# Kernel tuning notes

Measured on AMD Instinct MI355X. Metric: run time of the kernel, lower is better.

Reference implementation:

```python
import jax, jax.numpy as jnp
import numpy as np

# Module/config constants (match init_kwargs and torch forward defaults, octaves=8)
H, W, B = 1024, 1024, 16
OCTAVES = 8
PERSISTENCE = 0.5
LACUNARITY = 2.0
EXPONENT = 4.0
SCALE = 100.0
EVOLUTION = 0.1
FRAME = 0
BRIGHTNESS = 0.0
CONTRAST = 0.0
MIN_CLAMP = 0.0
MAX_CLAMP = 1.0
P_COUNT = max(H, W) ** 2  # permutation table size (doubled via concat)


def _fade(t):
    # 6t^5 - 15t^4 + 10t^3, Horner form
    return t * t * t * (t * (t * 6.0 - 15.0) + 10.0)


def _lerp(t, a, b):
    return a + t * (b - a)


def _grad(h, x, y, z):
    h = h & 15
    u = jnp.where(h < 8, x, y)
    v = jnp.where(h < 4, y, jnp.where((h == 12) | (h == 14), x, z))
    return jnp.where((h & 1) == 0, u, -u) + jnp.where((h & 2) == 0, v, -v)


def _noise(x, y, z, p):
    # classic 3D Perlin noise; x:(1,W), y:(H,1), z:(1,) broadcast to (H,W)
    Xi = (jnp.floor(x) % 255).astype(jnp.int32)
    Yi = (jnp.floor(y) % 255).astype(jnp.int32)
    Zi = (jnp.floor(z) % 255).astype(jnp.int32)
    xf = x - jnp.floor(x)
    yf = y - jnp.floor(y)
    zf = z - jnp.floor(z)
    u = _fade(xf)
    v = _fade(yf)
    w = _fade(zf)
    A = p[Xi] + Yi            # (H,W)
    AA = p[A] + Zi
    AB = p[A + 1] + Zi
    Bc = p[Xi + 1] + Yi
    BA = p[Bc] + Zi
    BB = p[Bc + 1] + Zi
    x1 = _lerp(u, _grad(p[AA], xf, yf, zf), _grad(p[BA], xf - 1, yf, zf))
    x2 = _lerp(u, _grad(p[AB], xf, yf - 1, zf), _grad(p[BB], xf - 1, yf - 1, zf))
    x3 = _lerp(u, _grad(p[AA + 1], xf, yf, zf - 1), _grad(p[BA + 1], xf - 1, yf, zf - 1))
    x4 = _lerp(u, _grad(p[AB + 1], xf, yf - 1, zf - 1), _grad(p[BB + 1], xf - 1, yf - 1, zf - 1))
    return _lerp(w, _lerp(v, x1, x2), _lerp(v, x3, x4))


def _forward(p_all, X, Y, Z):
    xs = jnp.arange(W, dtype=jnp.float32)[None, :] + X  # (1,W)
    ys = jnp.arange(H, dtype=jnp.float32)[:, None] + Y  # (H,1)

    def one_image(p, b):
        z0 = EVOLUTION * b + Z + FRAME  # (1,)
        acc = jnp.zeros((H, W), jnp.float32)
        for o in range(OCTAVES):  # small fixed loop over octaves
            freq = LACUNARITY ** o
            amp = PERSISTENCE ** o
            nz = (z0 + FRAME * EVOLUTION) / SCALE * freq
            n = _noise(xs / SCALE * freq, ys / SCALE * freq, nz, p)
            # noise * amp**exponent accumulated with weight amp -> amp**(exponent+1)
            acc = acc + n * np.float32(amp ** EXPONENT * amp)
        mn, mx = acc.min(), acc.max()
        img = (acc - mn) / (mx - mn) * (MAX_CLAMP - MIN_CLAMP) + MIN_CLAMP
        # second range_normalize(x) with None targets is the identity
        return (img + BRIGHTNESS) * (1.0 + CONTRAST)

    imgs = jax.vmap(one_image)(p_all, jnp.arange(B, dtype=jnp.float32))  # (B,H,W)
    return imgs[..., None]  # (B,H,W,1)


def setup_inputs() -> dict:
    key = jax.random.key(0)
    keys = jax.random.split(key, B)
    perm = jax.vmap(lambda k: jax.random.permutation(k, P_COUNT))(keys).astype(jnp.int32)
    p_all = jnp.concatenate([perm, perm], axis=1)  # (B, 2*P_COUNT), torch .repeat(2)
    kx, ky, kz = jax.random.split(jax.random.fold_in(key, 1), 3)
    X = jax.random.uniform(kx, (1,), jnp.float32, 0.0, 1000.0)
    Y = jax.random.uniform(ky, (1,), jnp.float32, 0.0, 1000.0)
    Z = jax.random.uniform(kz, (1,), jnp.float32, 0.0, 100.0)
    return {"p_all": p_all, "X": X, "Y": Y, "Z": Z}


def reference(p_all, X, Y, Z):
    return _forward(p_all, X, Y, Z)
```

## Files before the change

kernel.cpp:

```cpp
#include <hip/hip_runtime.h>


#define HW  1048576
#define PSTRIDE 2097152
#define PBS 1049088
#define OCT 4
#define RPB 8

struct ZTab { float zf, w; int Zi, pad; float w0, w1, wz0, wz1; };

__device__ __forceinline__ float fadef(float t) {
    return t * t * t * (t * (t * 6.0f - 15.0f) + 10.0f);
}
__device__ __forceinline__ void gdec(int h, float& a, float& cy, float& cz) {
    float s1 = (h & 1) ? -1.f : 1.f;
    float s2 = (h & 2) ? -1.f : 1.f;
    bool  vx = (h == 12) || (h == 14);
    a  = ((h < 8) ? s1 : 0.f) + (vx ? s2 : 0.f);
    cy = ((h >= 8) ? s1 : 0.f) + ((h < 4) ? s2 : 0.f);
    cz = (h >= 4 && !vx) ? s2 : 0.f;
}

__constant__ const float AW[8] = {
    1.0f, 0.03125f, 9.765625e-4f, 3.0517578125e-5f,
    9.5367431640625e-7f, 2.9802322387695312e-8f,
    9.313225746154785e-10f, 2.9103830456733704e-11f
};

__global__ void ppf_k0(const float* __restrict__ Z, ZTab* __restrict__ zs) {
    int t = threadIdx.x;
    if (t < 128) {
        int b = t >> 3, o = t & 7;
        float z0 = 0.1f * (float)b + Z[0];
        float freq = (float)(1 << o);
        float nz = (z0 / 100.0f) * freq;
        float fz = floorf(nz);
        ZTab zt;
        zt.Zi = ((int)fz) % 255;
        zt.zf = nz - fz;
        zt.w  = fadef(zt.zf);
        zt.pad = 0;
        zt.w0 = 1.0f - zt.w;
        zt.w1 = zt.w;
        zt.wz0 = zt.w0 * zt.zf;
        zt.wz1 = zt.w1 * (zt.zf - 1.0f);
        zs[t] = zt;
    }
}

__global__ void ppf_k0b(const int* __restrict__ p_all, unsigned char* __restrict__ pb) {
    int idx = blockIdx.x * 256 + threadIdx.x;
    int b = blockIdx.y;
    if (idx < PBS / 4) {
        int4 v = ((const int4*)(p_all + (size_t)b * PSTRIDE))[idx];
        uchar4 o;
        o.x = (unsigned char)(v.x & 15);
        o.y = (unsigned char)(v.y & 15);
        o.z = (unsigned char)(v.z & 15);
        o.w = (unsigned char)(v.w & 15);
        ((uchar4*)(pb + (size_t)b * PBS))[idx] = o;
    }
}

template <int USE_PB>
__global__ void ppf_k1(const int* __restrict__ p_all, const unsigned char* __restrict__ pb,
                       const ZTab* __restrict__ zs, unsigned char* __restrict__ G) {
    int i = threadIdx.x;
    int j = blockIdx.x;
    int b = blockIdx.y;
    const int* p = p_all + (size_t)b * PSTRIDE;
    const unsigned char* pbb = pb + (size_t)b * PBS;
    int pi = p[i];
    int q  = p[pi + j];
    size_t gbase = (size_t)b * OCT * 65536 + (size_t)j * 256 + i;
#pragma unroll
    for (int o = 0; o < OCT; o++) {
        int Zi = zs[b * 8 + o].Zi;
        int h0, h1;
        if (USE_PB) {
            h0 = pbb[q + Zi];
            h1 = pbb[q + Zi + 1];
        } else {
            h0 = p[q + Zi] & 15;
            h1 = p[q + Zi + 1] & 15;
        }
        G[gbase + (size_t)o * 65536] = (unsigned char)(h0 | (h1 << 4));
    }
}

__launch_bounds__(256, 8)
__global__ void ppf_k2(const unsigned char* __restrict__ G,
                       const ZTab* __restrict__ zs,
                       const float* __restrict__ X, const float* __restrict__ Y,
                       float* __restrict__ out, float2* __restrict__ pmm) {
    __shared__ __align__(16) float2 CT[2][OCT * 256];
    __shared__ float red[8];

    const int tid = threadIdx.x;
    const int bx = blockIdx.x, b = blockIdx.y;
    const float X0 = X[0], Y0 = Y[0];

    float zw0[OCT], zw1[OCT], zwz0[OCT], zwz1[OCT];
#pragma unroll
    for (int o = 0; o < OCT; o++) {
        ZTab z = zs[b * 8 + o];
        zw0[o] = z.w0; zw1[o] = z.w1; zwz0[o] = z.wz0; zwz1[o] = z.wz1;
    }

    float txs[4];
#pragma unroll
    for (int i = 0; i < 4; i++) txs[i] = ((float)(tid + 256 * i) + X0) * 0.01f;

    float mnr = 1e30f, mxr = -1e30f;
    int cur = 0;

    for (int rr = 0; rr < RPB; rr++) {
        const int r = bx * RPB + rr;
        const float ty = ((float)r + Y0) * 0.01f;

#pragma unroll
        for (int o = 0; o < OCT; o++) {
            float y  = ty * (float)(1 << o);
            float fy = floorf(y);
            float yf = y - fy, ym1 = yf - 1.0f;
            float v  = fadef(yf);
            int iy = (int)fy;
            int Yi = (iy >= 255) ? iy - 255 : iy;
            const unsigned char* gro = G + (((size_t)(b * OCT + o)) << 16)
                                         + (unsigned)Yi * 256u + tid;
            int byt0 = gro[0];
            int byt1 = gro[256];
            float a0, cy0, cz0, a1, cy1, cz1;
            gdec(byt0 & 15, a0, cy0, cz0);
            gdec(byt0 >> 4, a1, cy1, cz1);
            float A_0  = fmaf(zw1[o],  a1,  zw0[o] * a0);
            float CY_0 = fmaf(zw1[o],  cy1, zw0[o] * cy0);
            float CZ_0 = fmaf(zwz1[o], cz1, zwz0[o] * cz0);
            gdec(byt1 & 15, a0, cy0, cz0);
            gdec(byt1 >> 4, a1, cy1, cz1);
            float A_1  = fmaf(zw1[o],  a1,  zw0[o] * a0);
            float CY_1 = fmaf(zw1[o],  cy1, zw0[o] * cy0);
            float CZ_1 = fmaf(zwz1[o], cz1, zwz0[o] * cz0);
            float CA = A_0 + v * (A_1 - A_0);
            float B0 = fmaf(CY_0, yf,  CZ_0);
            float B1 = fmaf(CY_1, ym1, CZ_1);
            float CB = B0 + v * (B1 - B0);
            float aw = AW[o];
            CT[cur][o * 256 + tid] = make_float2(CA * aw, CB * aw);
        }
        __syncthreads();

        float accv[4] = {0.f, 0.f, 0.f, 0.f};
#pragma unroll
        for (int o = 0; o < OCT; o++) {
            const float fr = (float)(1 << o);
            const float2* cto = CT[cur] + o * 256;
            float xfv[4], uv[4];
            float2 c0v[4], c1v[4];
#pragma unroll
            for (int i = 0; i < 4; i++) {
                float x  = txs[i] * fr;
                float fx = floorf(x);
                float xf = x - fx;
                int  ix  = (int)fx;
                int  s   = (ix >> 8) + (ix & 255);
                s -= (s >= 255) ? 255 : 0;
                xfv[i] = xf;
                uv[i]  = fadef(xf);
                c0v[i] = cto[s];
                c1v[i] = cto[s + 1];
            }
#pragma unroll
            for (int i = 0; i < 4; i++) {
                float P = fmaf(c0v[i].x, xfv[i], c0v[i].y);
                float Q = fmaf(c1v[i].x, xfv[i] - 1.0f, c1v[i].y);
                accv[i] += fmaf(uv[i], Q - P, P);
            }
        }

        size_t obase = ((size_t)b << 20) + ((size_t)r << 10) + tid;
#pragma unroll
        for (int i = 0; i < 4; i++) out[obase + 256 * i] = accv[i];
        mnr = fminf(mnr, fminf(fminf(accv[0], accv[1]), fminf(accv[2], accv[3])));
        mxr = fmaxf(mxr, fmaxf(fmaxf(accv[0], accv[1]), fmaxf(accv[2], accv[3])));

        cur ^= 1;
    }

#pragma unroll
    for (int off = 32; off > 0; off >>= 1) {
        mnr = fminf(mnr, __shfl_down(mnr, off));
        mxr = fmaxf(mxr, __shfl_down(mxr, off));
    }
    if ((tid & 63) == 0) { red[2 * (tid >> 6)] = mnr; red[2 * (tid >> 6) + 1] = mxr; }
    __syncthreads();
    if (tid == 0) {
        float mn = fminf(fminf(red[0], red[2]), fminf(red[4], red[6]));
        float mx = fmaxf(fmaxf(red[1], red[3]), fmaxf(red[5], red[7]));
        pmm[b * 128 + bx] = make_float2(mn, mx);
    }
}

__global__ void ppf_k2b(const float2* __restrict__ pmm, float* __restrict__ mmf) {
    int b = blockIdx.x, t = threadIdx.x;
    __shared__ float s[4];
    float2 v = pmm[b * 128 + t];
    float mn = v.x, mx = v.y;
#pragma unroll
    for (int off = 32; off > 0; off >>= 1) {
        mn = fminf(mn, __shfl_down(mn, off));
        mx = fmaxf(mx, __shfl_down(mx, off));
    }
    if ((t & 63) == 0) { s[(t >> 6) * 2] = mn; s[(t >> 6) * 2 + 1] = mx; }
    __syncthreads();
    if (t == 0) {
        mn = fminf(s[0], s[2]);
        mx = fmaxf(s[1], s[3]);
        mmf[2 * b]     = mn;
        mmf[2 * b + 1] = 1.0f / (mx - mn);
    }
}

__global__ void ppf_k3(float* __restrict__ out, const float* __restrict__ mmf) {
    int b = blockIdx.y;
    int idx = blockIdx.x * 256 + threadIdx.x;
    float mn = mmf[2 * b];
    float s  = mmf[2 * b + 1];
    float4* o4 = (float4*)(out + (size_t)b * HW);
    float4 v = o4[idx];
    v.x = (v.x - mn) * s;
    v.y = (v.y - mn) * s;
    v.z = (v.z - mn) * s;
    v.w = (v.w - mn) * s;
    o4[idx] = v;
}

extern "C" void kernel_launch(void* const* d_in, const int* in_sizes, int n_in,
                              void* d_out, int out_size, void* d_ws, size_t ws_size,
                              hipStream_t stream) {
    const int*   p_all = (const int*)d_in[0];
    const float* X     = (const float*)d_in[1];
    const float* Y     = (const float*)d_in[2];
    const float* Z     = (const float*)d_in[3];
    float* out = (float*)d_out;
    char* ws = (char*)d_ws;

    const size_t GSZ = (size_t)16 * OCT * 65536;
    const size_t OFF_PB = GSZ;
    const size_t OFF_ZS_FULL = OFF_PB + (size_t)16 * PBS;
    const size_t NEED_FULL   = OFF_ZS_FULL + 8192 + 4096 + 16384;
    bool full = (ws_size >= NEED_FULL);
    size_t off_zs = full ? OFF_ZS_FULL : OFF_PB;

    unsigned char* G  = (unsigned char*)ws;
    unsigned char* pb = (unsigned char*)(ws + OFF_PB);
    ZTab*   zs        = (ZTab*)  (ws + off_zs);
    float*  mmf       = (float*) (ws + off_zs + 8192);
    float2* pmm       = (float2*)(ws + off_zs + 8192 + 4096);

    ppf_k0<<<1, 128, 0, stream>>>(Z, zs);
    if (full) {
        ppf_k0b<<<dim3(1025, 16), 256, 0, stream>>>(p_all, pb);
        ppf_k1<1><<<dim3(256, 16), 256, 0, stream>>>(p_all, pb, zs, G);
    } else {
        ppf_k1<0><<<dim3(256, 16), 256, 0, stream>>>(p_all, pb, zs, G);
    }
    ppf_k2<<<dim3(128, 16), 256, 0, stream>>>(G, zs, X, Y, out, pmm);
    ppf_k2b<<<16, 128, 0, stream>>>(pmm, mmf);
    ppf_k3<<<dim3(1024, 16), 256, 0, stream>>>(out, mmf);
}
```

Before: 367.5 us.

## Pack hash pairs, interleave octave bytes, drop modulo wrap, fuse min-max finalize

```diff
diff --git a/kernel.cpp b/kernel.cpp
--- a/kernel.cpp
+++ b/kernel.cpp
@@ -48,48 +48,49 @@
     }
 }
 
-__global__ void ppf_k0b(const int* __restrict__ p_all, unsigned char* __restrict__ pb) {
+__global__ void ppf_k0b(const int* __restrict__ p_all, unsigned char* __restrict__ pbp) {
     int idx = blockIdx.x * 256 + threadIdx.x;
     int b = blockIdx.y;
     if (idx < PBS / 4) {
-        int4 v = ((const int4*)(p_all + (size_t)b * PSTRIDE))[idx];
+        const int* p = p_all + (size_t)b * PSTRIDE;
+        int4 v = ((const int4*)p)[idx];
+        int n4 = p[idx * 4 + 4];
         uchar4 o;
-        o.x = (unsigned char)(v.x & 15);
-        o.y = (unsigned char)(v.y & 15);
-        o.z = (unsigned char)(v.z & 15);
-        o.w = (unsigned char)(v.w & 15);
-        ((uchar4*)(pb + (size_t)b * PBS))[idx] = o;
-    }
-}
-
-template <int USE_PB>
-__global__ void ppf_k1(const int* __restrict__ p_all, const unsigned char* __restrict__ pb,
-                       const ZTab* __restrict__ zs, unsigned char* __restrict__ G) {
-    int i = threadIdx.x;
-    int j = blockIdx.x;
+        o.x = (unsigned char)((v.x & 15) | ((v.y & 15) << 4));
+        o.y = (unsigned char)((v.y & 15) | ((v.z & 15) << 4));
+        o.z = (unsigned char)((v.z & 15) | ((v.w & 15) << 4));
+        o.w = (unsigned char)((v.w & 15) | ((n4 & 15) << 4));
+        ((uchar4*)(pbp + (size_t)b * PBS))[idx] = o;
+    }
+}
+
+template <int USE_PBP>
+__global__ void ppf_k1(const int* __restrict__ p_all, const unsigned char* __restrict__ pbp,
+                       const ZTab* __restrict__ zs, unsigned* __restrict__ G2) {
+    int j = threadIdx.x;
+    int i = blockIdx.x;
     int b = blockIdx.y;
     const int* p = p_all + (size_t)b * PSTRIDE;
-    const unsigned char* pbb = pb + (size_t)b * PBS;
     int pi = p[i];
     int q  = p[pi + j];
-    size_t gbase = (size_t)b * OCT * 65536 + (size_t)j * 256 + i;
+    const unsigned char* pp = pbp + (size_t)b * PBS;
+    unsigned w = 0;
 #pragma unroll
     for (int o = 0; o < OCT; o++) {
         int Zi = zs[b * 8 + o].Zi;
-        int h0, h1;
-        if (USE_PB) {
-            h0 = pbb[q + Zi];
-            h1 = pbb[q + Zi + 1];
+        unsigned byt;
+        if (USE_PBP) {
+            byt = pp[q + Zi];
         } else {
-            h0 = p[q + Zi] & 15;
-            h1 = p[q + Zi + 1] & 15;
+            byt = (unsigned)((p[q + Zi] & 15) | ((p[q + Zi + 1] & 15) << 4));
         }
-        G[gbase + (size_t)o * 65536] = (unsigned char)(h0 | (h1 << 4));
-    }
+        w |= byt << (8 * o);
+    }
+    G2[((size_t)b << 16) + ((unsigned)j << 8) + (unsigned)i] = w;
 }
 
 __launch_bounds__(256, 8)
-__global__ void ppf_k2(const unsigned char* __restrict__ G,
+__global__ void ppf_k2(const unsigned* __restrict__ G2,
                        const ZTab* __restrict__ zs,
                        const float* __restrict__ X, const float* __restrict__ Y,
                        float* __restrict__ out, float2* __restrict__ pmm) {
@@ -111,6 +112,8 @@
 #pragma unroll
     for (int i = 0; i < 4; i++) txs[i] = ((float)(tid + 256 * i) + X0) * 0.01f;
 
+    const unsigned char* gb = (const unsigned char*)G2 + ((size_t)b << 18);
+
     float mnr = 1e30f, mxr = -1e30f;
     int cur = 0;
 
@@ -124,12 +127,10 @@
             float fy = floorf(y);
             float yf = y - fy, ym1 = yf - 1.0f;
             float v  = fadef(yf);
-            int iy = (int)fy;
-            int Yi = (iy >= 255) ? iy - 255 : iy;
-            const unsigned char* gro = G + (((size_t)(b * OCT + o)) << 16)
-                                         + (unsigned)Yi * 256u + tid;
+            int Yi = (int)fy;
+            const unsigned char* gro = gb + ((((unsigned)Yi << 8) + tid) << 2) + o;
             int byt0 = gro[0];
-            int byt1 = gro[256];
+            int byt1 = gro[1024];
             float a0, cy0, cz0, a1, cy1, cz1;
             gdec(byt0 & 15, a0, cy0, cz0);
             gdec(byt0 >> 4, a1, cy1, cz1);
@@ -162,9 +163,7 @@
                 float x  = txs[i] * fr;
                 float fx = floorf(x);
                 float xf = x - fx;
-                int  ix  = (int)fx;
-                int  s   = (ix >> 8) + (ix & 255);
-                s -= (s >= 255) ? 255 : 0;
+                int  s   = (int)fx;
                 xfv[i] = xf;
                 uv[i]  = fadef(xf);
                 c0v[i] = cto[s];
@@ -201,37 +200,37 @@
     }
 }
 
-__global__ void ppf_k2b(const float2* __restrict__ pmm, float* __restrict__ mmf) {
-    int b = blockIdx.x, t = threadIdx.x;
-    __shared__ float s[4];
-    float2 v = pmm[b * 128 + t];
-    float mn = v.x, mx = v.y;
+__global__ void ppf_k3(float* __restrict__ out, const float2* __restrict__ pmm) {
+    __shared__ float sred[8];
+    __shared__ float sbc[2];
+    int b = blockIdx.y;
+    int tid = threadIdx.x;
+
+    float mn = 1e30f, mx = -1e30f;
+    if (tid < 128) { float2 v = pmm[b * 128 + tid]; mn = v.x; mx = v.y; }
 #pragma unroll
     for (int off = 32; off > 0; off >>= 1) {
         mn = fminf(mn, __shfl_down(mn, off));
         mx = fmaxf(mx, __shfl_down(mx, off));
     }
-    if ((t & 63) == 0) { s[(t >> 6) * 2] = mn; s[(t >> 6) * 2 + 1] = mx; }
+    if ((tid & 63) == 0) { sred[2 * (tid >> 6)] = mn; sred[2 * (tid >> 6) + 1] = mx; }
     __syncthreads();
-    if (t == 0) {
-        mn = fminf(s[0], s[2]);
-        mx = fmaxf(s[1], s[3]);
-        mmf[2 * b]     = mn;
-        mmf[2 * b + 1] = 1.0f / (mx - mn);
-    }
-}
-
-__global__ void ppf_k3(float* __restrict__ out, const float* __restrict__ mmf) {
-    int b = blockIdx.y;
-    int idx = blockIdx.x * 256 + threadIdx.x;
-    float mn = mmf[2 * b];
-    float s  = mmf[2 * b + 1];
+    if (tid == 0) {
+        mn = fminf(fminf(sred[0], sred[2]), fminf(sred[4], sred[6]));
+        mx = fmaxf(fmaxf(sred[1], sred[3]), fmaxf(sred[5], sred[7]));
+        sbc[0] = mn;
+        sbc[1] = 1.0f / (mx - mn);
+    }
+    __syncthreads();
+    float bmn = sbc[0], bs = sbc[1];
+
+    int idx = blockIdx.x * 256 + tid;
     float4* o4 = (float4*)(out + (size_t)b * HW);
     float4 v = o4[idx];
-    v.x = (v.x - mn) * s;
-    v.y = (v.y - mn) * s;
-    v.z = (v.z - mn) * s;
-    v.w = (v.w - mn) * s;
+    v.x = (v.x - bmn) * bs;
+    v.y = (v.y - bmn) * bs;
+    v.z = (v.z - bmn) * bs;
+    v.w = (v.w - bmn) * bs;
     o4[idx] = v;
 }
 
@@ -245,27 +244,25 @@
     float* out = (float*)d_out;
     char* ws = (char*)d_ws;
 
-    const size_t GSZ = (size_t)16 * OCT * 65536;
-    const size_t OFF_PB = GSZ;
-    const size_t OFF_ZS_FULL = OFF_PB + (size_t)16 * PBS;
-    const size_t NEED_FULL   = OFF_ZS_FULL + 8192 + 4096 + 16384;
+    const size_t GSZ = (size_t)16 * 65536 * 4;
+    const size_t OFF_PBP = GSZ;
+    const size_t OFF_ZS_FULL = OFF_PBP + (size_t)16 * PBS;
+    const size_t NEED_FULL   = OFF_ZS_FULL + 8192 + 16384;
     bool full = (ws_size >= NEED_FULL);
-    size_t off_zs = full ? OFF_ZS_FULL : OFF_PB;
-
-    unsigned char* G  = (unsigned char*)ws;
-    unsigned char* pb = (unsigned char*)(ws + OFF_PB);
-    ZTab*   zs        = (ZTab*)  (ws + off_zs);
-    float*  mmf       = (float*) (ws + off_zs + 8192);
-    float2* pmm       = (float2*)(ws + off_zs + 8192 + 4096);
+    size_t off_zs = full ? OFF_ZS_FULL : OFF_PBP;
+
+    unsigned* G2       = (unsigned*)ws;
+    unsigned char* pbp = (unsigned char*)(ws + OFF_PBP);
+    ZTab*   zs         = (ZTab*)  (ws + off_zs);
+    float2* pmm        = (float2*)(ws + off_zs + 8192);
 
     ppf_k0<<<1, 128, 0, stream>>>(Z, zs);
     if (full) {
-        ppf_k0b<<<dim3(1025, 16), 256, 0, stream>>>(p_all, pb);
-        ppf_k1<1><<<dim3(256, 16), 256, 0, stream>>>(p_all, pb, zs, G);
+        ppf_k0b<<<dim3(1025, 16), 256, 0, stream>>>(p_all, pbp);
+        ppf_k1<1><<<dim3(256, 16), 256, 0, stream>>>(p_all, pbp, zs, G2);
     } else {
-        ppf_k1<0><<<dim3(256, 16), 256, 0, stream>>>(p_all, pb, zs, G);
-    }
-    ppf_k2<<<dim3(128, 16), 256, 0, stream>>>(G, zs, X, Y, out, pmm);
-    ppf_k2b<<<16, 128, 0, stream>>>(pmm, mmf);
-    ppf_k3<<<dim3(1024, 16), 256, 0, stream>>>(out, mmf);
-}
+        ppf_k1<0><<<dim3(256, 16), 256, 0, stream>>>(p_all, pbp, zs, G2);
+    }
+    ppf_k2<<<dim3(128, 16), 256, 0, stream>>>(G2, zs, X, Y, out, pmm);
+    ppf_k3<<<dim3(1024, 16), 256, 0, stream>>>(out, pmm);
+}
```

Result: faster. 332.9 us (-9.4%).
